# Optimization experiments

Measured on AMD Instinct MI355X. Metric: run time of the kernel, lower is better.

The kernel has to match this reference:

```python
import jax, jax.numpy as jnp
import numpy as np

NUM_EXPERTS = 64
TOP_K = 2
TEMPERATURE = 1.0
MOMENTUM = 0.9


def _l2norm(x, axis=-1):
    # torch F.normalize: x / max(||x||, eps)
    n = jnp.linalg.norm(x, axis=axis, keepdims=True)
    return x / jnp.maximum(n, 1e-12)


def setup_inputs() -> dict:
    key = jax.random.key(0)
    k1, k2 = jax.random.split(key)
    hidden_states = jax.random.normal(k1, (4, 4096, 2048), dtype=jnp.float32)
    centers = _l2norm(jax.random.normal(k2, (NUM_EXPERTS, 2048), dtype=jnp.float32))
    return {"hidden_states": hidden_states, "centers": centers}


def reference(hidden_states, centers):
    B, T, H = hidden_states.shape
    flat = hidden_states.reshape(-1, H).astype(jnp.float32)  # [N, H]
    N = flat.shape[0]

    # cosine-similarity logits
    reps_n = _l2norm(flat)
    centers_n = _l2norm(centers)
    temp = jnp.maximum(jnp.float32(TEMPERATURE), 1e-6)
    logits = (reps_n @ centers_n.T) / temp  # [N, E]

    probs = jax.nn.softmax(logits, axis=-1)
    top_w, top_ids = jax.lax.top_k(probs, TOP_K)  # [N, k]
    top_w = top_w / (jnp.sum(top_w, axis=-1, keepdims=True) + 1e-9)

    # EMA center update from top-1 routed expert (training+update path)
    route = top_ids[:, 0]  # [N]
    sums = jax.ops.segment_sum(flat, route, num_segments=NUM_EXPERTS)  # [E, H]
    counts = jax.ops.segment_sum(jnp.ones((N, 1), jnp.float32), route,
                                 num_segments=NUM_EXPERTS)  # [E, 1]
    means = sums / (counts + 1e-6)
    updated = _l2norm(MOMENTUM * centers + (1.0 - MOMENTUM) * means)
    new_centers = jnp.where(counts > 0, updated, centers)

    top_ids = top_ids.reshape(B, T, TOP_K)
    top_w = top_w.reshape(B, T, TOP_K)
    return top_ids, top_w, new_centers
```

## Files before the change

### kernel.cpp

```cpp
#include <hip/hip_runtime.h>
#include <math.h>

#define NTOK 16384
#define HDIM 2048
#define NEXP 64
#define KK   32
#define TAU  5e-5f
#define MAXB 2048
#define KP2  40
#define LTS2 68

typedef __attribute__((ext_vector_type(8))) short short8;
typedef __attribute__((ext_vector_type(4))) float f32x4;
typedef __attribute__((ext_vector_type(2))) unsigned int uint2v;


__global__ __launch_bounds__(256)
void zero_kernel(float* p, int n) {
  int i = blockIdx.x * 256 + threadIdx.x;
  if (i < n) p[i] = 0.0f;
}

__device__ __forceinline__ float block_reduce_sum(float v, float* red) {
  #pragma unroll
  for (int o = 32; o > 0; o >>= 1) v += __shfl_down(v, o, 64);
  int lane = threadIdx.x & 63;
  int wid  = threadIdx.x >> 6;
  if (lane == 0) red[wid] = v;
  __syncthreads();
  float s = red[0] + red[1] + red[2] + red[3];
  __syncthreads();
  return s;
}

__device__ __forceinline__ double block_reduce_sum_f64(double v, double* red) {
  const int tid = threadIdx.x;
  red[tid] = v;
  __syncthreads();
  if (tid < 128) red[tid] += red[tid + 128];
  __syncthreads();
  if (tid < 64)  red[tid] += red[tid + 64];
  __syncthreads();
  double s = 0.0;
  if (tid < 64) {
    s = red[tid];
    #pragma unroll
    for (int o = 32; o > 0; o >>= 1) s += __shfl_down(s, o, 64);
  }
  if (tid == 0) red[0] = s;
  __syncthreads();
  s = red[0];
  __syncthreads();
  return s;
}

__global__ __launch_bounds__(256)
void cnorm_kernel(const float* __restrict__ c, float* __restrict__ inv_nc) {
  __shared__ float red[4];
  int e = blockIdx.x;
  float ss = 0.f;
  #pragma unroll
  for (int j = 0; j < 8; ++j) {
    float v = c[e * HDIM + threadIdx.x + j * 256];
    ss += v * v;
  }
  float tot = block_reduce_sum(ss, red);
  if (threadIdx.x == 0) inv_nc[e] = 1.0f / fmaxf(sqrtf(tot), 1e-12f);
}

__global__ __launch_bounds__(256)
void cprep_kernel(const float* __restrict__ c, float* __restrict__ inv_nc,
                  float* __restrict__ bn, unsigned short* __restrict__ cbh,
                  unsigned short* __restrict__ cbl, int* __restrict__ zr,
                  int* __restrict__ cnt) {
  __shared__ float red[4];
  __shared__ double redd[256];
  __shared__ float s_nc;
  const int e = blockIdx.x;
  const int tid = threadIdx.x;
  if (e == 0 && tid < 128) zr[tid] = 0;
  if (e == 1 && tid < 64)  cnt[tid] = 0;
  const float* cr = c + (size_t)e * HDIM;
  float ss = 0.f;
  double acc = 0.0;
  #pragma unroll
  for (int j = 0; j < 8; ++j) {
    float v = cr[tid + j * 256];
    ss += v * v;
    double dv = (double)v;
    acc += dv * dv;
  }
  float tot = block_reduce_sum(ss, red);
  double cn = block_reduce_sum_f64(acc, redd);
  if (tid == 0) {
    inv_nc[e] = 1.0f / fmaxf(sqrtf(tot), 1e-12f);
    s_nc = (float)fmax(sqrt(cn), 1e-12);
  }
  __syncthreads();
  const double nc = (double)s_nc;
  #pragma unroll
  for (int j = 0; j < 8; ++j) {
    const int k = tid + j * 256;
    const float v = cr[k];
    bn[(size_t)e * HDIM + k] = (float)((double)v / nc);
    unsigned u = __float_as_uint(v);
    unsigned h = u & 0xffff0000u;
    float r = v - __uint_as_float(h);
    cbh[(size_t)e * HDIM + k] = (unsigned short)(u >> 16);
    cbl[(size_t)e * HDIM + k] = (unsigned short)(__float_as_uint(r) >> 16);
  }
}

__device__ __forceinline__ void cvt2(float v0, float v1, unsigned &hi, unsigned &lo) {
  unsigned u0 = __float_as_uint(v0);
  unsigned u1 = __float_as_uint(v1);
  unsigned h0 = u0 & 0xffff0000u;
  unsigned h1 = u1 & 0xffff0000u;
  float r0 = v0 - __uint_as_float(h0);
  float r1 = v1 - __uint_as_float(h1);
  hi = (u0 >> 16) | h1;
  lo = (__float_as_uint(r0) >> 16) | (__float_as_uint(r1) & 0xffff0000u);
}

__global__ __launch_bounds__(256)
void gemm_part(const float* __restrict__ x,
               const unsigned short* __restrict__ cbh,
               const unsigned short* __restrict__ cbl,
               float* __restrict__ lp, float* __restrict__ xnp) {
  __shared__ __align__(16) unsigned short smem[10240];
  unsigned short (*Ah)[KP2] = (unsigned short (*)[KP2])(smem);
  unsigned short (*Al)[KP2] = (unsigned short (*)[KP2])(smem + 2560);
  unsigned short (*Bh)[KP2] = (unsigned short (*)[KP2])(smem + 5120);
  unsigned short (*Bl)[KP2] = (unsigned short (*)[KP2])(smem + 7680);

  const int tid  = threadIdx.x;
  const int mt   = blockIdx.x >> 3;
  const int ks   = blockIdx.x & 7;
  const int t0   = mt * 64;
  const int kb   = ks * 256;
  const int sr   = tid >> 2;
  const int sq   = (tid & 3) * 8;
  const int lane = tid & 63;
  const int w    = tid >> 6;
  const int tw   = (w & 1) * 32;
  const int ew   = (w >> 1) * 32;
  const int fr   = lane & 15;
  const int fk   = (lane >> 4) * 8;

  const float*          xrow  = x   + (size_t)(t0 + sr) * HDIM + kb + sq;
  const unsigned short* bhrow = cbh + (size_t)sr * HDIM + kb + sq;
  const unsigned short* blrow = cbl + (size_t)sr * HDIM + kb + sq;

  f32x4 xp0, xp1;
  short8 bhp, blp;
  float nacc = 0.f;

  xp0 = *(const f32x4*)(xrow);
  xp1 = *(const f32x4*)(xrow + 4);
  bhp = *(const short8*)(bhrow);
  blp = *(const short8*)(blrow);

  f32x4 acc[2][2];
  #pragma unroll
  for (int mi = 0; mi < 2; ++mi)
    #pragma unroll
    for (int ni = 0; ni < 2; ++ni)
      acc[mi][ni] = (f32x4){0.f, 0.f, 0.f, 0.f};

  for (int it = 0; it < 8; ++it) {
    __syncthreads();
    {
      unsigned h01, l01, h23, l23, h45, l45, h67, l67;
      cvt2(xp0.x, xp0.y, h01, l01);
      cvt2(xp0.z, xp0.w, h23, l23);
      cvt2(xp1.x, xp1.y, h45, l45);
      cvt2(xp1.z, xp1.w, h67, l67);
      *(uint2v*)&Ah[sr][sq]     = (uint2v){h01, h23};
      *(uint2v*)&Ah[sr][sq + 4] = (uint2v){h45, h67};
      *(uint2v*)&Al[sr][sq]     = (uint2v){l01, l23};
      *(uint2v*)&Al[sr][sq + 4] = (uint2v){l45, l67};
      nacc += xp0.x*xp0.x + xp0.y*xp0.y + xp0.z*xp0.z + xp0.w*xp0.w
            + xp1.x*xp1.x + xp1.y*xp1.y + xp1.z*xp1.z + xp1.w*xp1.w;
      *(short8*)&Bh[sr][sq] = bhp;
      *(short8*)&Bl[sr][sq] = blp;
    }
    __syncthreads();
    if (it < 7) {
      const int o = (it + 1) * KK;
      xp0 = *(const f32x4*)(xrow + o);
      xp1 = *(const f32x4*)(xrow + o + 4);
      bhp = *(const short8*)(bhrow + o);
      blp = *(const short8*)(blrow + o);
    }
    short8 ah0 = *(const short8*)&Ah[tw + fr][fk];
    short8 ah1 = *(const short8*)&Ah[tw + 16 + fr][fk];
    short8 al0 = *(const short8*)&Al[tw + fr][fk];
    short8 al1 = *(const short8*)&Al[tw + 16 + fr][fk];
    #pragma unroll
    for (int ni = 0; ni < 2; ++ni) {
      short8 bh = *(const short8*)&Bh[ew + ni * 16 + fr][fk];
      short8 bl = *(const short8*)&Bl[ew + ni * 16 + fr][fk];
      acc[0][ni] = __builtin_amdgcn_mfma_f32_16x16x32_bf16(ah0, bh, acc[0][ni], 0, 0, 0);
      acc[0][ni] = __builtin_amdgcn_mfma_f32_16x16x32_bf16(ah0, bl, acc[0][ni], 0, 0, 0);
      acc[0][ni] = __builtin_amdgcn_mfma_f32_16x16x32_bf16(al0, bh, acc[0][ni], 0, 0, 0);
      acc[1][ni] = __builtin_amdgcn_mfma_f32_16x16x32_bf16(ah1, bh, acc[1][ni], 0, 0, 0);
      acc[1][ni] = __builtin_amdgcn_mfma_f32_16x16x32_bf16(ah1, bl, acc[1][ni], 0, 0, 0);
      acc[1][ni] = __builtin_amdgcn_mfma_f32_16x16x32_bf16(al1, bh, acc[1][ni], 0, 0, 0);
    }
  }

  float s = nacc;
  s += __shfl_xor(s, 1, 64);
  s += __shfl_xor(s, 2, 64);
  if ((tid & 3) == 0) xnp[ks * NTOK + t0 + sr] = s;

  __syncthreads();
  float* lt = (float*)smem;
  const int tloc = tw + (lane >> 4) * 4;
  #pragma unroll
  for (int mi = 0; mi < 2; ++mi)
    #pragma unroll
    for (int ni = 0; ni < 2; ++ni)
      *(f32x4*)&lt[(ew + ni * 16 + fr) * LTS2 + tloc + mi * 16] = acc[mi][ni];
  __syncthreads();
  #pragma unroll
  for (int n = 0; n < 16; ++n) {
    const int f = tid + n * 256;
    const int e = f >> 6;
    const int t = f & 63;
    lp[(size_t)(ks * NEXP + e) * NTOK + t0 + t] = lt[e * LTS2 + t];
  }
}

__global__ __launch_bounds__(64)
void softmax2_kernel(const float* __restrict__ lp, const float* __restrict__ xnp,
                     const float* __restrict__ inv_nc, float* __restrict__ out,
                     int* __restrict__ route, int* __restrict__ nflag,
                     int* __restrict__ flags, int* __restrict__ cursor,
                     int* __restrict__ cnt, int* __restrict__ bucket,
                     int* __restrict__ posa) {
  __shared__ float snc[NEXP];
  const int tid = threadIdx.x;
  snc[tid] = inv_nc[tid];
  __syncthreads();
  const int t = blockIdx.x * 64 + tid;
  float xs2 = 0.f;
  #pragma unroll
  for (int k = 0; k < 8; ++k) xs2 += xnp[k * NTOK + t];
  const float inv_nx = 1.0f / fmaxf(sqrtf(xs2), 1e-12f);
  float lv[NEXP];
  #pragma unroll
  for (int e = 0; e < NEXP; ++e) {
    float a = 0.f;
    #pragma unroll
    for (int k = 0; k < 8; ++k)
      a += lp[(size_t)(k * NEXP + e) * NTOK + t];
    lv[e] = a * snc[e] * inv_nx;
  }
  float m1 = -1e30f, m2 = -1e30f, m3 = -1e30f;
  int i1 = 0, i2 = 0;
  #pragma unroll
  for (int e = 0; e < NEXP; ++e) {
    float l = lv[e];
    if (l > m1)      { m3 = m2; m2 = m1; i2 = i1; m1 = l; i1 = e; }
    else if (l > m2) { m3 = m2; m2 = l; i2 = e; }
    else if (l > m3) { m3 = l; }
  }
  float Z = 0.f;
  #pragma unroll
  for (int e = 0; e < NEXP; ++e) Z += expf(lv[e] - m1);
  const float p1w = 1.0f / Z;
  const float p2w = expf(m2 - m1) / Z;
  const float s2  = p1w + p2w + 1e-9f;
  out[t * 2 + 0] = (float)i1;
  out[t * 2 + 1] = (float)i2;
  out[2 * NTOK + t * 2 + 0] = p1w / s2;
  out[2 * NTOK + t * 2 + 1] = p2w / s2;
  route[t] = i1;
  const int p = atomicAdd(&cursor[i1], 1);
  atomicAdd(&cnt[i1], 1);
  if (p < MAXB) bucket[i1 * MAXB + p] = t;
  posa[t] = p;
  if ((m1 - m2) < TAU || (m2 - m3) < TAU) {
    int idx = atomicAdd(nflag, 1);
    flags[idx] = t;
  }
}

__global__ __launch_bounds__(256)
void refine_np_kernel(const float* __restrict__ x, const float* __restrict__ bn,
                      float* __restrict__ out, int* __restrict__ route,
                      const int* __restrict__ nflag, const int* __restrict__ flags,
                      int* __restrict__ cursor, int* __restrict__ cnt,
                      int* __restrict__ bucket, int* __restrict__ posa) {
  __shared__ float a_lds[HDIM];
  __shared__ double redd[256];
  __shared__ float lf[NEXP];
  __shared__ float s_nx;
  const int tid  = threadIdx.x;
  const int lane = tid & 63;
  const int w    = tid >> 6;
  const int n = *nflag;
  for (int j = blockIdx.x; j < n; j += gridDim.x) {
    const int t = flags[j];
    const float* xr = x + (size_t)t * HDIM;
    double xacc = 0.0;
    #pragma unroll
    for (int i = 0; i < 8; ++i) {
      double v = (double)xr[tid + 256 * i];
      xacc += v * v;
    }
    double xn = block_reduce_sum_f64(xacc, redd);
    if (tid == 0) s_nx = (float)fmax(sqrt(xn), 1e-12);
    __syncthreads();
    const double nx = (double)s_nx;
    #pragma unroll
    for (int i = 0; i < 8; ++i) {
      int k = tid + 256 * i;
      a_lds[k] = (float)((double)xr[k] / nx);
    }
    __syncthreads();
    #pragma unroll 1
    for (int ei = 0; ei < 16; ++ei) {
      const int e = w * 16 + ei;
      const float* br = bn + (size_t)e * HDIM;
      double d = 0.0;
      #pragma unroll 8
      for (int i = 0; i < 32; ++i) {
        int k = lane + 64 * i;
        d += (double)a_lds[k] * (double)br[k];
      }
      #pragma unroll
      for (int o = 32; o > 0; o >>= 1) d += __shfl_down(d, o, 64);
      if (lane == 0) lf[e] = (float)d;
    }
    __syncthreads();
    if (tid == 0) {
      float m32 = lf[0];
      for (int ee = 1; ee < NEXP; ++ee) m32 = fmaxf(m32, lf[ee]);
      float ex[NEXP];
      for (int ee = 0; ee < NEXP; ++ee)
        ex[ee] = (float)exp((double)(lf[ee] - m32));
      float r[8];
      #pragma unroll
      for (int q = 0; q < 8; ++q) r[q] = ex[q];
      for (int i = 8; i < NEXP; i += 8)
        #pragma unroll
        for (int q = 0; q < 8; ++q) r[q] += ex[i + q];
      const float Z = ((r[0] + r[1]) + (r[2] + r[3])) + ((r[4] + r[5]) + (r[6] + r[7]));
      float p1 = -1.f, p2 = -1.f;
      int i1 = 0, i2 = 0;
      for (int ee = 0; ee < NEXP; ++ee) {
        float p = ex[ee] / Z;
        if (p > p1)      { p2 = p1; i2 = i1; p1 = p; i1 = ee; }
        else if (p > p2) { p2 = p; i2 = ee; }
      }
      const float s = (p1 + p2) + 1e-9f;
      out[t * 2 + 0] = (float)i1;
      out[t * 2 + 1] = (float)i2;
      out[2 * NTOK + t * 2 + 0] = p1 / s;
      out[2 * NTOK + t * 2 + 1] = p2 / s;
      const int old = route[t];
      if (i1 != old) {
        const int p_old = posa[t];
        if (p_old < MAXB) bucket[old * MAXB + p_old] = -1;
        atomicSub(&cnt[old], 1);
        const int p = atomicAdd(&cursor[i1], 1);
        atomicAdd(&cnt[i1], 1);
        if (p < MAXB) bucket[i1 * MAXB + p] = t;
        posa[t] = p;
        route[t] = i1;
      }
    }
    __syncthreads();
  }
}

__global__ __launch_bounds__(64)
void refine_np_slow(const float* __restrict__ x, const float* __restrict__ c,
                    float* __restrict__ out, int* __restrict__ route,
                    const int* __restrict__ nflag, const int* __restrict__ flags) {
  __shared__ float lf[NEXP];
  const int e = threadIdx.x;
  const int n = *nflag;
  for (int j = blockIdx.x; j < n; j += gridDim.x) {
    const int t = flags[j];
    const float* xr = x + (size_t)t * HDIM;
    const float* cr = c + (size_t)e * HDIM;
    double xn = 0.0, cn = 0.0;
    for (int k = 0; k < HDIM; ++k) {
      double xv = (double)xr[k];
      double cv = (double)cr[k];
      xn += xv * xv;
      cn += cv * cv;
    }
    const float nx32 = (float)fmax(sqrt(xn), 1e-12);
    const float nc32 = (float)fmax(sqrt(cn), 1e-12);
    double d = 0.0;
    for (int k = 0; k < HDIM; ++k) {
      float a = (float)((double)xr[k] / (double)nx32);
      float b = (float)((double)cr[k] / (double)nc32);
      d += (double)a * (double)b;
    }
    lf[e] = (float)d;
    __syncthreads();
    if (e == 0) {
      float m32 = lf[0];
      for (int ee = 1; ee < NEXP; ++ee) m32 = fmaxf(m32, lf[ee]);
      float ex[NEXP];
      for (int ee = 0; ee < NEXP; ++ee)
        ex[ee] = (float)exp((double)(lf[ee] - m32));
      float r[8];
      #pragma unroll
      for (int q = 0; q < 8; ++q) r[q] = ex[q];
      for (int i = 8; i < NEXP; i += 8)
        #pragma unroll
        for (int q = 0; q < 8; ++q) r[q] += ex[i + q];
      const float Z = ((r[0] + r[1]) + (r[2] + r[3])) + ((r[4] + r[5]) + (r[6] + r[7]));
      float p1 = -1.f, p2 = -1.f;
      int i1 = 0, i2 = 0;
      for (int ee = 0; ee < NEXP; ++ee) {
        float p = ex[ee] / Z;
        if (p > p1)      { p2 = p1; i2 = i1; p1 = p; i1 = ee; }
        else if (p > p2) { p2 = p; i2 = ee; }
      }
      const float s = (p1 + p2) + 1e-9f;
      out[t * 2 + 0] = (float)i1;
      out[t * 2 + 1] = (float)i2;
      out[2 * NTOK + t * 2 + 0] = p1 / s;
      out[2 * NTOK + t * 2 + 1] = p2 / s;
      route[t] = i1;
    }
    __syncthreads();
  }
}

__global__ __launch_bounds__(256)
void segsum_part(const float* __restrict__ x, const int* __restrict__ cursor,
                 const int* __restrict__ bucket, float* __restrict__ psum) {
  __shared__ f32x4 part[4][64];
  const int e   = blockIdx.x >> 5;
  const int hc  = (blockIdx.x >> 2) & 7;
  const int ts  = blockIdx.x & 3;
  const int hb  = hc * 256;
  const int tid = threadIdx.x;
  const int rg  = tid >> 6;
  const int cc  = tid & 63;
  int n = cursor[e];
  if (n > MAXB) n = MAXB;
  const int nq = (n + 3) >> 2;
  const int lo = ts * nq;
  const int hi = min(lo + nq, n);
  const int* bk = bucket + e * MAXB;
  f32x4 a = (f32x4){0.f, 0.f, 0.f, 0.f};
  #pragma unroll 4
  for (int i = lo + rg; i < hi; i += 4) {
    const int r = bk[i];
    if (r >= 0) a += *(const f32x4*)(x + (size_t)r * HDIM + hb + cc * 4);
  }
  part[rg][cc] = a;
  __syncthreads();
  if (tid < 64) {
    f32x4 s = part[0][tid] + part[1][tid] + part[2][tid] + part[3][tid];
    *(f32x4*)&psum[(size_t)(ts * NEXP + e) * HDIM + hb + tid * 4] = s;
  }
}

__global__ __launch_bounds__(256)
void finalize4_kernel(const float* __restrict__ c, const float* __restrict__ psum,
                      const int* __restrict__ counts, float* __restrict__ out) {
  __shared__ float red[4];
  const int e = blockIdx.x;
  const int tid = threadIdx.x;
  const float cnt = (float)counts[e];
  const float minv = 1.0f / (cnt + 1e-6f);
  float u[8], cv[8];
  float ss = 0.f;
  #pragma unroll
  for (int j = 0; j < 8; ++j) {
    int h = tid + j * 256;
    cv[j] = c[e * HDIM + h];
    float sm = psum[(size_t)(0 * NEXP + e) * HDIM + h]
             + psum[(size_t)(1 * NEXP + e) * HDIM + h]
             + psum[(size_t)(2 * NEXP + e) * HDIM + h]
             + psum[(size_t)(3 * NEXP + e) * HDIM + h];
    float mean = sm * minv;
    u[j] = 0.9f * cv[j] + 0.1f * mean;
    ss += u[j] * u[j];
  }
  float tot = block_reduce_sum(ss, red);
  float sc = 1.0f / fmaxf(sqrtf(tot), 1e-12f);
  const bool nz = cnt > 0.f;
  #pragma unroll
  for (int j = 0; j < 8; ++j) {
    int h = tid + j * 256;
    out[4 * NTOK + e * HDIM + h] = nz ? u[j] * sc : cv[j];
  }
}

__global__ __launch_bounds__(256)
void finalize_kernel(const float* __restrict__ c, const float* __restrict__ sums,
                     const int* __restrict__ counts, float* __restrict__ out) {
  __shared__ float red[4];
  const int e = blockIdx.x;
  const int tid = threadIdx.x;
  const float cnt = (float)counts[e];
  const float minv = 1.0f / (cnt + 1e-6f);
  float u[8], cv[8];
  float ss = 0.f;
  #pragma unroll
  for (int j = 0; j < 8; ++j) {
    int h = tid + j * 256;
    cv[j] = c[e * HDIM + h];
    float mean = sums[e * HDIM + h] * minv;
    u[j] = 0.9f * cv[j] + 0.1f * mean;
    ss += u[j] * u[j];
  }
  float tot = block_reduce_sum(ss, red);
  float sc = 1.0f / fmaxf(sqrtf(tot), 1e-12f);
  const bool nz = cnt > 0.f;
  #pragma unroll
  for (int j = 0; j < 8; ++j) {
    int h = tid + j * 256;
    out[4 * NTOK + e * HDIM + h] = nz ? u[j] * sc : cv[j];
  }
}

__global__ __launch_bounds__(256)
void router_kernel(const float* __restrict__ x, const float* __restrict__ c,
                   const float* __restrict__ inv_nc, float* __restrict__ out,
                   int* __restrict__ route, int* __restrict__ nflag,
                   int* __restrict__ flags) {
  __shared__ __align__(16) float xs[64][36];
  __shared__ float lgs[64][67];
  const int tid  = threadIdx.x;
  const int lane = tid & 63;
  const int w    = tid >> 6;
  const int t0   = blockIdx.x * 64;
  const int e0   = __builtin_amdgcn_readfirstlane(w * 16);
  const float* cb = c + (size_t)e0 * HDIM;
  const int st = tid >> 3;
  const int sk = (tid & 7) * 4;
  float acc[16];
  #pragma unroll
  for (int e = 0; e < 16; ++e) acc[e] = 0.f;
  float nacc = 0.f;
  float4 p0 = *(const float4*)&x[(size_t)(t0 + st)      * HDIM + sk];
  float4 p1 = *(const float4*)&x[(size_t)(t0 + st + 32) * HDIM + sk];
  for (int k0 = 0; k0 < HDIM; k0 += 32) {
    __syncthreads();
    *(float4*)&xs[st][sk]      = p0;
    *(float4*)&xs[st + 32][sk] = p1;
    __syncthreads();
    const int kn = k0 + 32;
    if (kn < HDIM) {
      p0 = *(const float4*)&x[(size_t)(t0 + st)      * HDIM + kn + sk];
      p1 = *(const float4*)&x[(size_t)(t0 + st + 32) * HDIM + kn + sk];
    }
    float a[32];
    #pragma unroll
    for (int j = 0; j < 32; j += 4) {
      float4 v = *(const float4*)&xs[lane][j];
      a[j] = v.x; a[j+1] = v.y; a[j+2] = v.z; a[j+3] = v.w;
    }
    if (w == 0) {
      #pragma unroll
      for (int j = 0; j < 32; ++j) nacc += a[j] * a[j];
    }
    #pragma unroll
    for (int e = 0; e < 16; ++e) {
      const float* br = cb + (size_t)e * HDIM + k0;
      #pragma unroll
      for (int j = 0; j < 32; j += 4) {
        float4 bv = *(const float4*)&br[j];
        acc[e] += a[j]*bv.x + a[j+1]*bv.y + a[j+2]*bv.z + a[j+3]*bv.w;
      }
    }
  }
  #pragma unroll
  for (int e = 0; e < 16; ++e) lgs[lane][e0 + e] = acc[e] * inv_nc[e0 + e];
  __syncthreads();
  if (w == 0) {
    const float inv_nx = 1.0f / fmaxf(sqrtf(nacc), 1e-12f);
    float m1 = -1e30f, m2 = -1e30f, m3 = -1e30f;
    int i1 = 0, i2 = 0;
    for (int e = 0; e < NEXP; ++e) {
      float l = lgs[lane][e] * inv_nx;
      if (l > m1)      { m3 = m2; m2 = m1; i2 = i1; m1 = l; i1 = e; }
      else if (l > m2) { m3 = m2; m2 = l; i2 = e; }
      else if (l > m3) { m3 = l; }
    }
    float Z = 0.f;
    for (int e = 0; e < NEXP; ++e) Z += expf(lgs[lane][e] * inv_nx - m1);
    const float p1w = 1.0f / Z;
    const float p2w = expf(m2 - m1) / Z;
    const float s   = p1w + p2w + 1e-9f;
    const int tg = t0 + lane;
    out[tg * 2 + 0] = (float)i1;
    out[tg * 2 + 1] = (float)i2;
    out[2 * NTOK + tg * 2 + 0] = p1w / s;
    out[2 * NTOK + tg * 2 + 1] = p2w / s;
    route[tg] = i1;
    if ((m1 - m2) < TAU || (m2 - m3) < TAU) {
      int idx = atomicAdd(nflag, 1);
      flags[idx] = tg;
    }
  }
}

__global__ __launch_bounds__(512)
void segsum_kernel(const float* __restrict__ x, const int* __restrict__ route,
                   float* __restrict__ sums, int* __restrict__ counts) {
  __shared__ float ls[NEXP * 256];
  __shared__ int lcnt[NEXP];
  const int tid  = threadIdx.x;
  const int lane = tid & 63;
  const int w    = tid >> 6;
  const int hc   = blockIdx.x & 7;
  const int tg   = blockIdx.x >> 3;
  const int hb   = hc * 256;
  #pragma unroll
  for (int i = 0; i < 32; ++i) ls[tid + i * 512] = 0.f;
  if (tid < NEXP) lcnt[tid] = 0;
  __syncthreads();
  const int tbase = tg * 512 + w * 64;
  #pragma unroll 4
  for (int i = 0; i < 64; ++i) {
    const int t = tbase + i;
    const int e = route[t];
    const float* xr = x + (size_t)t * HDIM + hb + lane;
    #pragma unroll
    for (int j = 0; j < 4; ++j)
      atomicAdd(&ls[e * 256 + lane + 64 * j], xr[64 * j]);
    if (hc == 0 && lane == 0) atomicAdd(&lcnt[e], 1);
  }
  __syncthreads();
  #pragma unroll
  for (int i = tid; i < NEXP * 256; i += 512) {
    const int e = i >> 8, h = i & 255;
    atomicAdd(&sums[e * HDIM + hb + h], ls[i]);
  }
  if (hc == 0 && tid < NEXP && lcnt[tid] > 0) atomicAdd(&counts[tid], lcnt[tid]);
}

extern "C" void kernel_launch(void* const* d_in, const int* in_sizes, int n_in,
                              void* d_out, int out_size, void* d_ws, size_t ws_size,
                              hipStream_t stream) {
  const float* x = (const float*)d_in[0];
  const float* c = (const float*)d_in[1];
  float* out = (float*)d_out;
  float* ws = (float*)d_ws;

  float* inv_nc = ws;
  int*   cursor = (int*)(ws + 64);
  int*   nflag  = (int*)(ws + 128);
  int*   route  = (int*)(ws + 192);
  int*   flags  = (int*)(ws + 16576);
  float* sums   = ws + 32960;
  float* bn     = ws + 164032;
  unsigned short* cbh = (unsigned short*)(ws + 295104);
  unsigned short* cbl = (unsigned short*)(ws + 360640);
  int*   bucket = (int*)(ws + 426176);
  float* psum   = ws + 557248;
  int*   posa   = (int*)(ws + 1081536);
  int*   cnt    = (int*)(ws + 1097920);
  float* lp     = ws + 1097984;
  float* xnp    = ws + 9486592;

  const size_t NEED = 9617664ull * 4ull;
  if (ws_size >= NEED) {
    cprep_kernel<<<NEXP, 256, 0, stream>>>(c, inv_nc, bn, cbh, cbl, cursor, cnt);
    gemm_part<<<2048, 256, 0, stream>>>(x, cbh, cbl, lp, xnp);
    softmax2_kernel<<<NTOK / 64, 64, 0, stream>>>(lp, xnp, inv_nc, out, route,
                                                  nflag, flags, cursor, cnt, bucket, posa);
    refine_np_kernel<<<512, 256, 0, stream>>>(x, bn, out, route, nflag, flags,
                                              cursor, cnt, bucket, posa);
    segsum_part<<<2048, 256, 0, stream>>>(x, cursor, bucket, psum);
    finalize4_kernel<<<NEXP, 256, 0, stream>>>(c, psum, cnt, out);
  } else {
    zero_kernel<<<1, 256, 0, stream>>>(ws + 64, 128);
    zero_kernel<<<512, 256, 0, stream>>>(sums, 131072);
    cnorm_kernel<<<NEXP, 256, 0, stream>>>(c, inv_nc);
    router_kernel<<<NTOK / 64, 256, 0, stream>>>(x, c, inv_nc, out, route, nflag, flags);
    refine_np_slow<<<1024, 64, 0, stream>>>(x, c, out, route, nflag, flags);
    segsum_kernel<<<256, 512, 0, stream>>>(x, route, sums, cursor);
    finalize_kernel<<<NEXP, 256, 0, stream>>>(c, sums, cursor, out);
  }
}
```

Before: 339.1 us.

## Parallelize split-K partial logit reduction across eight waves in softmax kernel

The softmax kernel now launches 512 threads per 64-token block instead of 64. Eight waves each sum four K-split partials for a 16-expert slice and combine them through LDS, so the 512 strided partial-logit loads per token are spread across more wavefronts. Only the first wave then does top-k, softmax and the atomics. This adds LDS traffic and two barriers, and the seven other waves sit idle during the serial part.

```diff
diff --git a/kernel.cpp b/kernel.cpp
--- a/kernel.cpp
+++ b/kernel.cpp
@@ -232,58 +232,80 @@
   }
 }
 
-__global__ __launch_bounds__(64)
+__global__ __launch_bounds__(512)
 void softmax2_kernel(const float* __restrict__ lp, const float* __restrict__ xnp,
                      const float* __restrict__ inv_nc, float* __restrict__ out,
                      int* __restrict__ route, int* __restrict__ nflag,
                      int* __restrict__ flags, int* __restrict__ cursor,
                      int* __restrict__ cnt, int* __restrict__ bucket,
                      int* __restrict__ posa) {
+  __shared__ float lg[NEXP][68];
   __shared__ float snc[NEXP];
-  const int tid = threadIdx.x;
-  snc[tid] = inv_nc[tid];
-  __syncthreads();
-  const int t = blockIdx.x * 64 + tid;
-  float xs2 = 0.f;
-  #pragma unroll
-  for (int k = 0; k < 8; ++k) xs2 += xnp[k * NTOK + t];
-  const float inv_nx = 1.0f / fmaxf(sqrtf(xs2), 1e-12f);
-  float lv[NEXP];
-  #pragma unroll
-  for (int e = 0; e < NEXP; ++e) {
-    float a = 0.f;
-    #pragma unroll
-    for (int k = 0; k < 8; ++k)
-      a += lp[(size_t)(k * NEXP + e) * NTOK + t];
-    lv[e] = a * snc[e] * inv_nx;
-  }
-  float m1 = -1e30f, m2 = -1e30f, m3 = -1e30f;
-  int i1 = 0, i2 = 0;
-  #pragma unroll
-  for (int e = 0; e < NEXP; ++e) {
-    float l = lv[e];
-    if (l > m1)      { m3 = m2; m2 = m1; i2 = i1; m1 = l; i1 = e; }
-    else if (l > m2) { m3 = m2; m2 = l; i2 = e; }
-    else if (l > m3) { m3 = l; }
-  }
-  float Z = 0.f;
-  #pragma unroll
-  for (int e = 0; e < NEXP; ++e) Z += expf(lv[e] - m1);
-  const float p1w = 1.0f / Z;
-  const float p2w = expf(m2 - m1) / Z;
-  const float s2  = p1w + p2w + 1e-9f;
-  out[t * 2 + 0] = (float)i1;
-  out[t * 2 + 1] = (float)i2;
-  out[2 * NTOK + t * 2 + 0] = p1w / s2;
-  out[2 * NTOK + t * 2 + 1] = p2w / s2;
-  route[t] = i1;
-  const int p = atomicAdd(&cursor[i1], 1);
-  atomicAdd(&cnt[i1], 1);
-  if (p < MAXB) bucket[i1 * MAXB + p] = t;
-  posa[t] = p;
-  if ((m1 - m2) < TAU || (m2 - m3) < TAU) {
-    int idx = atomicAdd(nflag, 1);
-    flags[idx] = t;
+  const int tid  = threadIdx.x;
+  const int lane = tid & 63;
+  const int w    = tid >> 6;
+  const int kg   = w >> 2;
+  const int eg   = (w & 3) * 16;
+  const int t0   = blockIdx.x * 64;
+  const int t    = t0 + lane;
+  if (tid < NEXP) snc[tid] = inv_nc[tid];
+
+  float p[16];
+  const float* base = lp + (size_t)(kg * 4 * NEXP + eg) * NTOK + t;
+  #pragma unroll
+  for (int e = 0; e < 16; ++e) {
+    const float* q = base + (size_t)e * NTOK;
+    float a0 = q[0];
+    float a1 = q[(size_t)NEXP * NTOK];
+    float a2 = q[(size_t)2 * NEXP * NTOK];
+    float a3 = q[(size_t)3 * NEXP * NTOK];
+    p[e] = (a0 + a1) + (a2 + a3);
+  }
+  if (kg == 0) {
+    #pragma unroll
+    for (int e = 0; e < 16; ++e) lg[eg + e][lane] = p[e];
+  }
+  __syncthreads();
+  if (kg == 1) {
+    #pragma unroll
+    for (int e = 0; e < 16; ++e) lg[eg + e][lane] += p[e];
+  }
+  __syncthreads();
+
+  if (tid < 64) {
+    float xs2 = 0.f;
+    #pragma unroll
+    for (int k = 0; k < 8; ++k) xs2 += xnp[k * NTOK + t];
+    const float inv_nx = 1.0f / fmaxf(sqrtf(xs2), 1e-12f);
+    float m1 = -1e30f, m2 = -1e30f, m3 = -1e30f;
+    int i1 = 0, i2 = 0;
+    #pragma unroll
+    for (int e = 0; e < NEXP; ++e) {
+      float l = lg[e][lane] * snc[e] * inv_nx;
+      if (l > m1)      { m3 = m2; m2 = m1; i2 = i1; m1 = l; i1 = e; }
+      else if (l > m2) { m3 = m2; m2 = l; i2 = e; }
+      else if (l > m3) { m3 = l; }
+    }
+    float Z = 0.f;
+    #pragma unroll
+    for (int e = 0; e < NEXP; ++e)
+      Z += expf(lg[e][lane] * snc[e] * inv_nx - m1);
+    const float p1w = 1.0f / Z;
+    const float p2w = expf(m2 - m1) / Z;
+    const float s2  = p1w + p2w + 1e-9f;
+    out[t * 2 + 0] = (float)i1;
+    out[t * 2 + 1] = (float)i2;
+    out[2 * NTOK + t * 2 + 0] = p1w / s2;
+    out[2 * NTOK + t * 2 + 1] = p2w / s2;
+    route[t] = i1;
+    const int p0 = atomicAdd(&cursor[i1], 1);
+    atomicAdd(&cnt[i1], 1);
+    if (p0 < MAXB) bucket[i1 * MAXB + p0] = t;
+    posa[t] = p0;
+    if ((m1 - m2) < TAU || (m2 - m3) < TAU) {
+      int idx = atomicAdd(nflag, 1);
+      flags[idx] = t;
+    }
   }
 }
 
@@ -671,8 +693,8 @@
   if (ws_size >= NEED) {
     cprep_kernel<<<NEXP, 256, 0, stream>>>(c, inv_nc, bn, cbh, cbl, cursor, cnt);
     gemm_part<<<2048, 256, 0, stream>>>(x, cbh, cbl, lp, xnp);
-    softmax2_kernel<<<NTOK / 64, 64, 0, stream>>>(lp, xnp, inv_nc, out, route,
-                                                  nflag, flags, cursor, cnt, bucket, posa);
+    softmax2_kernel<<<NTOK / 64, 512, 0, stream>>>(lp, xnp, inv_nc, out, route,
+                                                   nflag, flags, cursor, cnt, bucket, posa);
     refine_np_kernel<<<512, 256, 0, stream>>>(x, bn, out, route, nflag, flags,
                                               cursor, cnt, bucket, posa);
     segsum_part<<<2048, 256, 0, stream>>>(x, cursor, bucket, psum);
```

Result: faster. 312.2 us (-7.9%).
